# Optimization experiments

Measured on AMD Instinct MI355X. Metric: run time of the kernel, lower is better.

## Reference

```python
import jax, jax.numpy as jnp
import numpy as np

B, N, D = 512, 500000, 128
K = 100


def setup_inputs() -> dict:
    key = jax.random.key(0)
    kq, kc = jax.random.split(key)
    queries = jax.random.normal(kq, (B, D), dtype=jnp.float32)
    candidates = jax.random.normal(kc, (N, D), dtype=jnp.float32)
    identifiers = jnp.arange(N, dtype=jnp.int32)
    return {
        "queries": queries,
        "candidates": candidates,
        "identifiers": identifiers,
        "num_candidates": K,
    }


def reference(queries, candidates, identifiers, num_candidates):
    # scores: [B, N] dense similarity matrix (dot product)
    scores = jnp.einsum("bd,nd->bn", queries, candidates)
    # top-k per query row
    values, indices = jax.lax.top_k(scores, num_candidates)  # [B, K] each
    top_ids = jnp.take(identifiers, indices, axis=0)          # [B, K]
    return values, top_ids
```

## Files before the change

kernel.cpp:

```cpp
#include <hip/hip_runtime.h>
#include <cfloat>


#define D_DIM 128
#define K_TOP 100
#define THRESH_SIGMA 3.25f
#define CAP_MAX 512
#define KEEP_MAXF 256
#define FGRID 512
#define TROWS 64

typedef short bf16x8 __attribute__((ext_vector_type(8)));
typedef float f32x4 __attribute__((ext_vector_type(4)));

__device__ __forceinline__ unsigned short f2bf(float x) {
    unsigned u = __float_as_uint(x);
    return (unsigned short)((u + 0x7FFFu + ((u >> 16) & 1u)) >> 16);
}

__device__ __forceinline__ unsigned long long make_key(float v, unsigned id) {
    unsigned vb = __float_as_uint(v);
    unsigned vm = (vb & 0x80000000u) ? ~vb : (vb | 0x80000000u);
    return ((unsigned long long)vm << 32) | (0xFFFFFFFFu - id);
}

template <int S>
__device__ inline void bitonic_sort_u64(unsigned long long* buf) {
    for (int k = 2; k <= S; k <<= 1) {
        for (int j = k >> 1; j > 0; j >>= 1) {
            __syncthreads();
            for (int i = threadIdx.x; i < S; i += blockDim.x) {
                int l = i ^ j;
                if (l > i) {
                    unsigned long long a = buf[i], b = buf[l];
                    bool sw = ((i & k) == 0) ? (a > b) : (a < b);
                    if (sw) { buf[i] = b; buf[l] = a; }
                }
            }
        }
    }
    __syncthreads();
}

__global__ void prep2_kernel(const float* __restrict__ Qm, float* __restrict__ thr,
                             int* __restrict__ cnt, int B) {
    int b = blockIdx.x * blockDim.x + threadIdx.x;
    if (b >= B) return;
    float s = 0.f;
    for (int d = 0; d < D_DIM; ++d) { float v = Qm[(size_t)b * D_DIM + d]; s = fmaf(v, v, s); }
    thr[b] = THRESH_SIGMA * sqrtf(s);
    cnt[b] = 0;
}

__global__ void qfrag_kernel(const float* __restrict__ Qm, uint4* __restrict__ qf,
                             int B, int nch) {
    int tid = blockIdx.x * blockDim.x + threadIdx.x;
    int total = nch * 8 * 4 * 64;
    if (tid >= total) return;
    int l  = tid & 63;
    int ks = (tid >> 6) & 3;
    int qb = (tid >> 8) & 7;
    int qch = tid >> 11;
    int qrow = qch * 128 + qb * 16 + (l & 15);
    int k0 = ks * 32 + (l >> 4) * 8;
    uint4 o = make_uint4(0u, 0u, 0u, 0u);
    if (qrow < B) {
        const float* src = Qm + (size_t)qrow * D_DIM + k0;
        unsigned r[4];
#pragma unroll
        for (int j = 0; j < 4; ++j)
            r[j] = (unsigned)f2bf(src[2 * j]) | ((unsigned)f2bf(src[2 * j + 1]) << 16);
        o = make_uint4(r[0], r[1], r[2], r[3]);
    }
    qf[tid] = o;
}

__global__ __launch_bounds__(256, 2) void mfma_filter_kernel(
    const float* __restrict__ cand, const bf16x8* __restrict__ qfrag,
    const float* __restrict__ thr, unsigned* __restrict__ idbuf,
    int* __restrict__ cnt, int N, int Bg, int cap, int nch, int ntiles) {
    __shared__ __align__(16) char cl[2][TROWS * 512];
    const int t = threadIdx.x;
    const int w = t >> 6;
    const int l = t & 63;

    const bool qv = (w < nch);
    const int qch = qv ? w : (nch > 0 ? nch - 1 : 0);
    bf16x8 bq[8][4];
#pragma unroll
    for (int qb = 0; qb < 8; ++qb)
#pragma unroll
        for (int ks = 0; ks < 4; ++ks)
            bq[qb][ks] = qfrag[((qch * 8 + qb) * 4 + ks) * 64 + l];
    float tvq[8];
#pragma unroll
    for (int qb = 0; qb < 8; ++qb) {
        int qg = qch * 128 + qb * 16 + (l & 15);
        tvq[qb] = (qv && qg < Bg) ? thr[qg] : 3.0e38f;
    }

    int tile = blockIdx.x;
    if (tile >= ntiles) return;

#define STAGE(BUFI, T)                                                              \
    do {                                                                            \
        int c0s = (T) * TROWS;                                                      \
        _Pragma("unroll")                                                           \
        for (int i = 0; i < 8; ++i) {                                               \
            int rl = (w * 8 + i) * 2 + (l >> 5);                                    \
            int gr = c0s + rl; if (gr > N - 1) gr = N - 1;                          \
            int ug = (l & 31) ^ (rl & 7);                                           \
            const float* srcp = cand + (size_t)gr * D_DIM + ug * 4;                 \
            __builtin_amdgcn_global_load_lds(                                       \
                (const __attribute__((address_space(1))) void*)srcp,                \
                (__attribute__((address_space(3))) void*)(&cl[BUFI][(w * 8 + i) * 1024]), \
                16, 0, 0);                                                          \
        }                                                                           \
    } while (0)

    STAGE(0, tile);
    int cur = 0;
#pragma unroll 1
    while (true) {
        int nxt = tile + FGRID;
        bool hn = (nxt < ntiles);
        if (hn) {
            STAGE(cur ^ 1, nxt);
            asm volatile("s_waitcnt vmcnt(8)" ::: "memory");
        } else {
            asm volatile("s_waitcnt vmcnt(0)" ::: "memory");
        }
        __builtin_amdgcn_s_barrier();

        {
            const char* bp = cl[cur];
            int c0 = tile * TROWS;
#pragma unroll
            for (int cb = 0; cb < 4; ++cb) {
                int r = cb * 16 + (l & 15);
                int sb = r * 512, s = r & 7;
                bf16x8 af[4];
#pragma unroll
                for (int ks = 0; ks < 4; ++ks) {
                    int u0 = ks * 8 + (l >> 4) * 2;
                    f32x4 f0 = *reinterpret_cast<const f32x4*>(bp + sb + ((u0 ^ s) << 4));
                    f32x4 f1 = *reinterpret_cast<const f32x4*>(bp + sb + (((u0 + 1) ^ s) << 4));
                    union { bf16x8 v; unsigned u[4]; } p;
                    p.u[0] = (__float_as_uint(f0[0]) >> 16) | (__float_as_uint(f0[1]) & 0xFFFF0000u);
                    p.u[1] = (__float_as_uint(f0[2]) >> 16) | (__float_as_uint(f0[3]) & 0xFFFF0000u);
                    p.u[2] = (__float_as_uint(f1[0]) >> 16) | (__float_as_uint(f1[1]) & 0xFFFF0000u);
                    p.u[3] = (__float_as_uint(f1[2]) >> 16) | (__float_as_uint(f1[3]) & 0xFFFF0000u);
                    af[ks] = p.v;
                }
                f32x4 acc[8];
#pragma unroll
                for (int qb = 0; qb < 8; ++qb) acc[qb] = (f32x4){0.f, 0.f, 0.f, 0.f};
#pragma unroll
                for (int ks = 0; ks < 4; ++ks) {
                    bf16x8 a = af[ks];
#pragma unroll
                    for (int qb = 0; qb < 8; ++qb)
                        acc[qb] = __builtin_amdgcn_mfma_f32_16x16x32_bf16(
                            a, bq[qb][ks], acc[qb], 0, 0, 0);
                }
#pragma unroll
                for (int qb = 0; qb < 8; ++qb) {
                    float tv = tvq[qb];
                    f32x4 a = acc[qb];
                    float m = fmaxf(fmaxf(a[0], a[1]), fmaxf(a[2], a[3]));
                    if (m > tv) {
                        int qg = qch * 128 + qb * 16 + (l & 15);
#pragma unroll
                        for (int rr = 0; rr < 4; ++rr) {
                            if (a[rr] > tv) {
                                int cid = c0 + cb * 16 + ((l >> 4) << 2) + rr;
                                if (cid < N) {
                                    int pos = atomicAdd(&cnt[qg], 1);
                                    if (pos < cap) idbuf[(size_t)qg * cap + pos] = (unsigned)cid;
                                }
                            }
                        }
                    }
                }
            }
        }

        if (!hn) break;
        __builtin_amdgcn_s_barrier();
        cur ^= 1; tile = nxt;
    }
#undef STAGE
}

__global__ void fallback_kernel(const float* __restrict__ Qm, const float* __restrict__ cand,
                                unsigned* __restrict__ idbuf, int* __restrict__ cnt,
                                int N, int cap) {
    int q = blockIdx.x;
    int c0 = cnt[q];
    if (c0 >= K_TOP && c0 <= cap) return;
    int keep = (cap < KEEP_MAXF) ? cap : KEEP_MAXF;

    __shared__ unsigned long long buf[2048];
    __shared__ float qrow[D_DIM];
    __shared__ int bn;
    __shared__ float theta;
    __shared__ int validn;
    for (int i = threadIdx.x; i < D_DIM; i += blockDim.x) qrow[i] = Qm[(size_t)q * D_DIM + i];
    for (int i = threadIdx.x; i < 2048; i += blockDim.x) buf[i] = 0ULL;
    if (threadIdx.x == 0) { bn = 0; theta = -3.0e38f; }
    __syncthreads();

    for (int base = 0; base < N; base += blockDim.x) {
        int c = base + threadIdx.x;
        if (c < N) {
            float s = 0.f;
            for (int d = 0; d < D_DIM; ++d) s = fmaf(qrow[d], cand[(size_t)c * D_DIM + d], s);
            if (s > theta) {
                int p = atomicAdd(&bn, 1);
                if (p < 2048) buf[p] = make_key(s, (unsigned)c);
            }
        }
        __syncthreads();
        if (bn > 2048 - 256 - 8) {
            bitonic_sort_u64<2048>(buf);
            unsigned long long kv = (threadIdx.x < (unsigned)keep) ? buf[2047 - threadIdx.x] : 0ULL;
            __syncthreads();
            for (int i = threadIdx.x; i < 2048; i += blockDim.x) buf[i] = 0ULL;
            __syncthreads();
            if (threadIdx.x < (unsigned)keep) buf[threadIdx.x] = kv;
            if ((int)threadIdx.x == keep - 1) {
                unsigned vm = (unsigned)(kv >> 32);
                unsigned vb = (vm & 0x80000000u) ? (vm ^ 0x80000000u) : ~vm;
                theta = __uint_as_float(vb) - 0.01f;
            }
            if (threadIdx.x == 0) bn = keep;
            __syncthreads();
        }
    }
    bitonic_sort_u64<2048>(buf);
    if (threadIdx.x == 0) validn = 0;
    __syncthreads();
    unsigned long long kv = (threadIdx.x < (unsigned)keep) ? buf[2047 - threadIdx.x] : 0ULL;
    if (kv != 0ULL) atomicAdd(&validn, 1);
    __syncthreads();
    if ((int)threadIdx.x < validn && threadIdx.x < (unsigned)keep) {
        unsigned id = 0xFFFFFFFFu - (unsigned)(kv & 0xFFFFFFFFu);
        if (id < (unsigned)N) idbuf[(size_t)q * cap + threadIdx.x] = id;
    }
    if (threadIdx.x == 0) cnt[q] = (validn < keep) ? validn : keep;
}

__device__ __forceinline__ float np_lane_chain(float q0, float b0v, float q1, float b1v,
                                               float q2, float b2v, float q3, float b3v,
                                               float acc) {
    float t = __fadd_rn(__fmul_rn(q3, b3v), acc);
    t = __fadd_rn(__fmul_rn(q2, b2v), t);
    t = __fadd_rn(__fmul_rn(q1, b1v), t);
    return __fadd_rn(__fmul_rn(q0, b0v), t);
}

__device__ __forceinline__ float np_score(const float* __restrict__ qrow,
                                          const float* __restrict__ crow) {
    float acc0 = 0.f, acc1 = 0.f, acc2 = 0.f, acc3 = 0.f;
#pragma unroll
    for (int d0 = 0; d0 < D_DIM; d0 += 16) {
        float4 b0 = *reinterpret_cast<const float4*>(crow + d0 + 0);
        float4 b1 = *reinterpret_cast<const float4*>(crow + d0 + 4);
        float4 b2 = *reinterpret_cast<const float4*>(crow + d0 + 8);
        float4 b3 = *reinterpret_cast<const float4*>(crow + d0 + 12);
        acc0 = np_lane_chain(qrow[d0 + 0], b0.x, qrow[d0 + 4], b1.x,
                             qrow[d0 + 8], b2.x, qrow[d0 + 12], b3.x, acc0);
        acc1 = np_lane_chain(qrow[d0 + 1], b0.y, qrow[d0 + 5], b1.y,
                             qrow[d0 + 9], b2.y, qrow[d0 + 13], b3.y, acc1);
        acc2 = np_lane_chain(qrow[d0 + 2], b0.z, qrow[d0 + 6], b1.z,
                             qrow[d0 + 10], b2.z, qrow[d0 + 14], b3.z, acc2);
        acc3 = np_lane_chain(qrow[d0 + 3], b0.w, qrow[d0 + 7], b1.w,
                             qrow[d0 + 11], b2.w, qrow[d0 + 15], b3.w, acc3);
    }
    return __fadd_rn(__fadd_rn(acc0, acc1), __fadd_rn(acc2, acc3));
}

__global__ __launch_bounds__(256) void select_kernel(
    const float* __restrict__ Qm, const float* __restrict__ cand,
    const unsigned* __restrict__ idbuf, const int* __restrict__ cnt,
    const int* __restrict__ ident, float* __restrict__ out, int N, int B, int cap) {
    __shared__ unsigned long long skey[CAP_MAX];
    __shared__ float qrow[D_DIM];
    int q = blockIdx.x;
    for (int i = threadIdx.x; i < D_DIM; i += blockDim.x) qrow[i] = Qm[(size_t)q * D_DIM + i];
    __syncthreads();

    int n = cnt[q]; if (n > cap) n = cap; if (n > CAP_MAX) n = CAP_MAX;
    for (int i = threadIdx.x; i < CAP_MAX; i += blockDim.x) {
        unsigned long long key = 0ULL;
        if (i < n) {
            unsigned id = idbuf[(size_t)q * cap + i];
            if (id < (unsigned)N) {
                float s = np_score(qrow, cand + (size_t)id * D_DIM);
                key = make_key(s, id);
            }
        }
        skey[i] = key;
    }

    bitonic_sort_u64<CAP_MAX>(skey);

    for (int t = threadIdx.x; t < K_TOP; t += blockDim.x) {
        unsigned long long key = skey[CAP_MAX - 1 - t];
        unsigned vm = (unsigned)(key >> 32);
        unsigned vb = (vm & 0x80000000u) ? (vm ^ 0x80000000u) : ~vm;
        unsigned id = 0xFFFFFFFFu - (unsigned)(key & 0xFFFFFFFFu);
        if (id >= (unsigned)N) id = 0;
        out[(size_t)q * K_TOP + t] = __uint_as_float(vb);
        out[(size_t)B * K_TOP + (size_t)q * K_TOP + t] = (float)ident[id];
    }
}

extern "C" void kernel_launch(void* const* d_in, const int* in_sizes, int n_in,
                              void* d_out, int out_size, void* d_ws, size_t ws_size,
                              hipStream_t stream) {
    const float* queries = (const float*)d_in[0];
    const float* cands   = (const float*)d_in[1];
    const int*   ident   = (const int*)d_in[2];
    const int B = in_sizes[0] / D_DIM;
    const int N = in_sizes[2];
    float* out = (float*)d_out;
    const int nch = (B + 127) >> 7;
    const int ntiles = (N + TROWS - 1) / TROWS;

    char* ws = (char*)d_ws;
    int*   cnt = (int*)ws;
    float* thr = (float*)(ws + 2048);
    uint4* qfrag = (uint4*)(ws + 4096);
    size_t ids_off = 4096 + (size_t)nch * 32768;
    unsigned* idbuf = (unsigned*)(ws + ids_off);
    int cap = CAP_MAX;
    if (ws_size > ids_off) {
        size_t fit = (ws_size - ids_off) / ((size_t)B * 4);
        if (fit < (size_t)cap) cap = (int)fit;
    } else cap = 1;
    if (cap < 1) cap = 1;

    prep2_kernel<<<(B + 255) / 256, 256, 0, stream>>>(queries, thr, cnt, B);
    int qft = nch * 2048;
    qfrag_kernel<<<(qft + 255) / 256, 256, 0, stream>>>(queries, qfrag, B, nch);

    int ngrp = (nch + 3) / 4;
    for (int g = 0; g < ngrp; ++g) {
        int nch_g = nch - g * 4; if (nch_g > 4) nch_g = 4;
        int B_g = B - g * 512; if (B_g > 512) B_g = 512;
        mfma_filter_kernel<<<FGRID, 256, 0, stream>>>(
            cands, (const bf16x8*)(qfrag + (size_t)g * 8192),
            thr + (size_t)g * 512, idbuf + (size_t)g * 512 * cap,
            cnt + (size_t)g * 512, N, B_g, cap, nch_g, ntiles);
    }

    fallback_kernel<<<B, 256, 0, stream>>>(queries, cands, idbuf, cnt, N, cap);

    select_kernel<<<B, 256, 0, stream>>>(queries, cands, idbuf, cnt, ident, out, N, B, cap);
}
```

Measured before the change: 165.6 us.

## Deepen filter kernel prefetch to four-stage ring with smaller tiles

Moves the candidate staging in the MFMA filter kernel from double buffering to a four-buffer ring. Tiles shrink from 64 to 32 rows and three tiles are kept in flight via global_load_lds, clamping past-the-end tiles to the last valid tile. It also swaps the bf16 truncation packing for a byte-permute builtin. The intent is to hide more global-memory latency and cut ALU work per packed value, at the cost of redundant loads at the tail and smaller MFMA work per barrier.

```diff
diff --git a/kernel.cpp b/kernel.cpp
--- a/kernel.cpp
+++ b/kernel.cpp
@@ -8,7 +8,7 @@
 #define CAP_MAX 512
 #define KEEP_MAXF 256
 #define FGRID 512
-#define TROWS 64
+#define TROWS 32
 
 typedef short bf16x8 __attribute__((ext_vector_type(8)));
 typedef float f32x4 __attribute__((ext_vector_type(4)));
@@ -16,6 +16,14 @@
 __device__ __forceinline__ unsigned short f2bf(float x) {
     unsigned u = __float_as_uint(x);
     return (unsigned short)((u + 0x7FFFu + ((u >> 16) & 1u)) >> 16);
+}
+
+__device__ __forceinline__ unsigned pack_hi16(unsigned hi, unsigned lo) {
+#if __has_builtin(__builtin_amdgcn_perm)
+    return __builtin_amdgcn_perm(hi, lo, 0x07060302u);
+#else
+    return (lo >> 16) | (hi & 0xFFFF0000u);
+#endif
 }
 
 __device__ __forceinline__ unsigned long long make_key(float v, unsigned id) {
@@ -79,10 +87,12 @@
     const float* __restrict__ cand, const bf16x8* __restrict__ qfrag,
     const float* __restrict__ thr, unsigned* __restrict__ idbuf,
     int* __restrict__ cnt, int N, int Bg, int cap, int nch, int ntiles) {
-    __shared__ __align__(16) char cl[2][TROWS * 512];
+    __shared__ __align__(16) char cl[4][TROWS * 512];
     const int t = threadIdx.x;
     const int w = t >> 6;
     const int l = t & 63;
+    const int lr = l & 15;
+    const int lk = l >> 4;
 
     const bool qv = (w < nch);
     const int qch = qv ? w : (nch > 0 ? nch - 1 : 0);
@@ -95,61 +105,59 @@
     float tvq[8];
 #pragma unroll
     for (int qb = 0; qb < 8; ++qb) {
-        int qg = qch * 128 + qb * 16 + (l & 15);
+        int qg = qch * 128 + qb * 16 + lr;
         tvq[qb] = (qv && qg < Bg) ? thr[qg] : 3.0e38f;
     }
 
-    int tile = blockIdx.x;
-    if (tile >= ntiles) return;
+    const int t0 = blockIdx.x;
+    if (t0 >= ntiles) return;
 
 #define STAGE(BUFI, T)                                                              \
     do {                                                                            \
         int c0s = (T) * TROWS;                                                      \
         _Pragma("unroll")                                                           \
-        for (int i = 0; i < 8; ++i) {                                               \
-            int rl = (w * 8 + i) * 2 + (l >> 5);                                    \
+        for (int i = 0; i < 4; ++i) {                                               \
+            int rl = (w * 4 + i) * 2 + (l >> 5);                                    \
             int gr = c0s + rl; if (gr > N - 1) gr = N - 1;                          \
             int ug = (l & 31) ^ (rl & 7);                                           \
             const float* srcp = cand + (size_t)gr * D_DIM + ug * 4;                 \
             __builtin_amdgcn_global_load_lds(                                       \
                 (const __attribute__((address_space(1))) void*)srcp,                \
-                (__attribute__((address_space(3))) void*)(&cl[BUFI][(w * 8 + i) * 1024]), \
+                (__attribute__((address_space(3))) void*)(&cl[BUFI][(w * 4 + i) * 1024]), \
                 16, 0, 0);                                                          \
         }                                                                           \
     } while (0)
-
-    STAGE(0, tile);
-    int cur = 0;
+#define CLAMPT(X) ((X) < ntiles ? (X) : (ntiles - 1))
+
+    STAGE(0, t0);
+    STAGE(1, CLAMPT(t0 + FGRID));
+    STAGE(2, CLAMPT(t0 + 2 * FGRID));
+
+    int it = 0;
 #pragma unroll 1
-    while (true) {
-        int nxt = tile + FGRID;
-        bool hn = (nxt < ntiles);
-        if (hn) {
-            STAGE(cur ^ 1, nxt);
-            asm volatile("s_waitcnt vmcnt(8)" ::: "memory");
-        } else {
-            asm volatile("s_waitcnt vmcnt(0)" ::: "memory");
-        }
+    for (int tile = t0; tile < ntiles; tile += FGRID, ++it) {
+        STAGE((it + 3) & 3, CLAMPT(tile + 3 * FGRID));
+        asm volatile("s_waitcnt vmcnt(12)" ::: "memory");
         __builtin_amdgcn_s_barrier();
 
         {
-            const char* bp = cl[cur];
+            const char* bp = cl[it & 3];
             int c0 = tile * TROWS;
 #pragma unroll
-            for (int cb = 0; cb < 4; ++cb) {
-                int r = cb * 16 + (l & 15);
+            for (int cb = 0; cb < 2; ++cb) {
+                int r = cb * 16 + lr;
                 int sb = r * 512, s = r & 7;
                 bf16x8 af[4];
 #pragma unroll
                 for (int ks = 0; ks < 4; ++ks) {
-                    int u0 = ks * 8 + (l >> 4) * 2;
+                    int u0 = ks * 8 + lk * 2;
                     f32x4 f0 = *reinterpret_cast<const f32x4*>(bp + sb + ((u0 ^ s) << 4));
                     f32x4 f1 = *reinterpret_cast<const f32x4*>(bp + sb + (((u0 + 1) ^ s) << 4));
                     union { bf16x8 v; unsigned u[4]; } p;
-                    p.u[0] = (__float_as_uint(f0[0]) >> 16) | (__float_as_uint(f0[1]) & 0xFFFF0000u);
-                    p.u[1] = (__float_as_uint(f0[2]) >> 16) | (__float_as_uint(f0[3]) & 0xFFFF0000u);
-                    p.u[2] = (__float_as_uint(f1[0]) >> 16) | (__float_as_uint(f1[1]) & 0xFFFF0000u);
-                    p.u[3] = (__float_as_uint(f1[2]) >> 16) | (__float_as_uint(f1[3]) & 0xFFFF0000u);
+                    p.u[0] = pack_hi16(__float_as_uint(f0[1]), __float_as_uint(f0[0]));
+                    p.u[1] = pack_hi16(__float_as_uint(f0[3]), __float_as_uint(f0[2]));
+                    p.u[2] = pack_hi16(__float_as_uint(f1[1]), __float_as_uint(f1[0]));
+                    p.u[3] = pack_hi16(__float_as_uint(f1[3]), __float_as_uint(f1[2]));
                     af[ks] = p.v;
                 }
                 f32x4 acc[8];
@@ -169,11 +177,11 @@
                     f32x4 a = acc[qb];
                     float m = fmaxf(fmaxf(a[0], a[1]), fmaxf(a[2], a[3]));
                     if (m > tv) {
-                        int qg = qch * 128 + qb * 16 + (l & 15);
+                        int qg = qch * 128 + qb * 16 + lr;
 #pragma unroll
                         for (int rr = 0; rr < 4; ++rr) {
                             if (a[rr] > tv) {
-                                int cid = c0 + cb * 16 + ((l >> 4) << 2) + rr;
+                                int cid = c0 + cb * 16 + (lk << 2) + rr;
                                 if (cid < N) {
                                     int pos = atomicAdd(&cnt[qg], 1);
                                     if (pos < cap) idbuf[(size_t)qg * cap + pos] = (unsigned)cid;
@@ -184,12 +192,10 @@
                 }
             }
         }
-
-        if (!hn) break;
         __builtin_amdgcn_s_barrier();
-        cur ^= 1; tile = nxt;
     }
 #undef STAGE
+#undef CLAMPT
 }
 
 __global__ void fallback_kernel(const float* __restrict__ Qm, const float* __restrict__ cand,
```

Measured after the change: 174.6 us. 5.4% more time.
